# Kernel tuning notes

Hardware: AMD Instinct MI355X
Metric: run time of the kernel (lower is better)

The kernel has to match this reference:

```python
import jax, jax.numpy as jnp
import numpy as np

N_NODES = 100000


def gcn_conv(x, edge_index, W, b):
    """PyG GCNConv: linear transform, add self-loops, sym-normalized scatter-add, bias."""
    n = x.shape[0]
    h = x @ W  # [N, out]
    loop = jnp.arange(n, dtype=edge_index.dtype)
    src = jnp.concatenate([edge_index[0], loop])
    dst = jnp.concatenate([edge_index[1], loop])
    deg = jax.ops.segment_sum(jnp.ones_like(dst, dtype=h.dtype), dst, num_segments=n)
    dinv = jnp.where(deg > 0, jax.lax.rsqrt(jnp.maximum(deg, 1.0)), 0.0)
    norm = dinv[src] * dinv[dst]  # [E+N]
    msg = norm[:, None] * h[src]  # gather + scale
    out = jax.ops.segment_sum(msg, dst, num_segments=n)  # scatter-add
    return out + b


def setup_inputs() -> dict:
    key = jax.random.key(0)
    k1, k2, k3, k4 = jax.random.split(key, 4)
    in_f, gnn_f, out_f = 128, 64, 40
    n_edges = 1600000
    x = jax.random.normal(k1, (N_NODES, in_f), dtype=jnp.float32)
    edge_index = jax.random.randint(k2, (2, n_edges), 0, N_NODES, dtype=jnp.int64)
    W1 = jax.random.normal(k3, (in_f, gnn_f), dtype=jnp.float32) * (in_f ** -0.5)
    b1 = jnp.zeros((gnn_f,), dtype=jnp.float32)
    W2 = jax.random.normal(k4, (gnn_f, out_f), dtype=jnp.float32) * (gnn_f ** -0.5)
    b2 = jnp.zeros((out_f,), dtype=jnp.float32)
    return {"x": x, "edge_index": edge_index, "W1": W1, "b1": b1, "W2": W2, "b2": b2}


def reference(x, edge_index, W1, b1, W2, b2):
    h = gcn_conv(x, edge_index, W1, b1)
    h = jax.nn.relu(h)  # Dropout is identity in eval mode
    out = gcn_conv(h, edge_index, W2, b2)
    return out
```

## Files before the change

### kernel.cpp

```cpp
#include <hip/hip_runtime.h>


__device__ inline float bflo(unsigned u) { return __uint_as_float(u << 16); }
__device__ inline float bfhi(unsigned u) { return __uint_as_float(u & 0xffff0000u); }
__device__ inline unsigned short f2bf(float x) {
    unsigned u = __float_as_uint(x);
    return (unsigned short)((u + 0x7fff + ((u >> 16) & 1)) >> 16);
}

#define NBINS 256
#define EPB   2048

__global__ __launch_bounds__(256) void p1_hist(const int* __restrict__ dst, int e,
                                               int nblk, int* __restrict__ hist_t) {
    __shared__ int h[NBINS];
    int tid = threadIdx.x;
    h[tid] = 0;
    __syncthreads();
    int base = blockIdx.x * EPB;
    #pragma unroll
    for (int j = 0; j < 8; ++j) {
        int idx = base + j * 256 + tid;
        if (idx < e) atomicAdd(&h[dst[idx] >> 9], 1);
    }
    __syncthreads();
    hist_t[tid * nblk + blockIdx.x] = h[tid];
}

__global__ __launch_bounds__(256) void scan_a(const int* __restrict__ in, int* __restrict__ part,
                                              int* __restrict__ aux, int n) {
    __shared__ int lds[256];
    int tid = threadIdx.x;
    int base = blockIdx.x * 1024 + tid * 4;
    int v0 = (base + 0 < n) ? in[base + 0] : 0;
    int v1 = (base + 1 < n) ? in[base + 1] : 0;
    int v2 = (base + 2 < n) ? in[base + 2] : 0;
    int v3 = (base + 3 < n) ? in[base + 3] : 0;
    int s = v0 + v1 + v2 + v3;
    lds[tid] = s;
    __syncthreads();
    for (int off = 1; off < 256; off <<= 1) {
        int t = (tid >= off) ? lds[tid - off] : 0;
        __syncthreads();
        lds[tid] += t;
        __syncthreads();
    }
    int excl = lds[tid] - s;
    if (base + 0 < n) part[base + 0] = excl;
    if (base + 1 < n) part[base + 1] = excl + v0;
    if (base + 2 < n) part[base + 2] = excl + v0 + v1;
    if (base + 3 < n) part[base + 3] = excl + v0 + v1 + v2;
    if (tid == 255) aux[blockIdx.x] = lds[255];
}

__global__ __launch_bounds__(256) void scan_b(int* __restrict__ aux, int nb) {
    __shared__ int lds[256];
    int tid = threadIdx.x;
    int v = (tid < nb) ? aux[tid] : 0;
    lds[tid] = v;
    __syncthreads();
    for (int off = 1; off < 256; off <<= 1) {
        int t = (tid >= off) ? lds[tid - off] : 0;
        __syncthreads();
        lds[tid] += t;
        __syncthreads();
    }
    if (tid < nb) aux[tid] = lds[tid] - v;
}

__global__ __launch_bounds__(256) void scan_c(int* __restrict__ data,
                                              const int* __restrict__ aux, int n) {
    int i = blockIdx.x * blockDim.x + threadIdx.x;
    if (i < n) data[i] += aux[i >> 10];
}

__global__ __launch_bounds__(256) void p1_scatter(const int* __restrict__ src,
                                                  const int* __restrict__ dst, int e,
                                                  int nblk, const int* __restrict__ off_t,
                                                  uint2* __restrict__ ebuf) {
    __shared__ int cur[NBINS];
    int tid = threadIdx.x;
    cur[tid] = off_t[tid * nblk + blockIdx.x];
    __syncthreads();
    int base = blockIdx.x * EPB;
    #pragma unroll
    for (int j = 0; j < 8; ++j) {
        int idx = base + j * 256 + tid;
        if (idx < e) {
            int d = dst[idx];
            int p = atomicAdd(&cur[d >> 9], 1);
            ebuf[p] = make_uint2((unsigned)src[idx], (unsigned)d);
        }
    }
}

__global__ __launch_bounds__(256) void p2_build(const uint2* __restrict__ ebuf,
                                                const int* __restrict__ off_t,
                                                int nblk, int e, int n, int nbg,
                                                int* __restrict__ row_off,
                                                int* __restrict__ ssrc,
                                                float* __restrict__ dinv) {
    __shared__ int cnt[512];
    __shared__ int s1[256];
    __shared__ int loc[512];
    int tid = threadIdx.x;
    int g = blockIdx.x;
    int node0 = g << 9;
    int nlocal = n - node0; if (nlocal > 512) nlocal = 512;

    int segstart = off_t[g * nblk];
    int segend   = (g + 1 < NBINS) ? off_t[(g + 1) * nblk] : e;

    cnt[tid] = 0; cnt[tid + 256] = 0;
    __syncthreads();

    for (int i = segstart + tid; i < segend; i += 256)
        atomicAdd(&cnt[ebuf[i].y - node0], 1);
    __syncthreads();

    int a0 = cnt[2 * tid], a1 = cnt[2 * tid + 1];
    int sp = a0 + a1;
    s1[tid] = sp;
    __syncthreads();
    for (int off = 1; off < 256; off <<= 1) {
        int t = (tid >= off) ? s1[tid - off] : 0;
        __syncthreads();
        s1[tid] += t;
        __syncthreads();
    }
    int excl = s1[tid] - sp;
    loc[2 * tid]     = excl;
    loc[2 * tid + 1] = excl + a0;
    __syncthreads();

    for (int l = tid; l < nlocal; l += 256) {
        row_off[node0 + l] = segstart + loc[l];
        dinv[node0 + l] = rsqrtf((float)cnt[l] + 1.0f);
    }
    if (g == nbg - 1 && tid == 0) row_off[n] = segend;
    __syncthreads();

    for (int i = segstart + tid; i < segend; i += 256) {
        uint2 p = ebuf[i];
        int r = atomicAdd(&loc[p.y - node0], 1);
        ssrc[segstart + r] = (int)p.x;
    }
}

template <int K, int M>
__global__ __launch_bounds__(256) void gemm_xw(const float* __restrict__ X,
                                               const float* __restrict__ W,
                                               const float* __restrict__ dinv,
                                               unsigned short* __restrict__ G, int n) {
    constexpr int KQ = K / 4;
    constexpr int SG = KQ + 1;
    __shared__ float4 xs[64 * SG];
    __shared__ float4 wt[64 * SG];

    const int tid = threadIdx.x;
    const int r0  = blockIdx.x * 64;

    for (int idx = tid; idx < 64 * KQ; idx += 256) {
        int m  = idx / KQ;
        int kq = idx & (KQ - 1);
        float4 v = make_float4(0.f, 0.f, 0.f, 0.f);
        if (m < M) {
            int k = kq * 4;
            v.x = W[(k + 0) * M + m];
            v.y = W[(k + 1) * M + m];
            v.z = W[(k + 2) * M + m];
            v.w = W[(k + 3) * M + m];
        }
        wt[m * SG + kq] = v;
    }
    for (int idx = tid; idx < 64 * KQ; idx += 256) {
        int row = idx / KQ;
        int kq  = idx & (KQ - 1);
        int rr  = r0 + row; rr = rr < n ? rr : n - 1;
        xs[row * SG + kq] = *reinterpret_cast<const float4*>(&X[(size_t)rr * K + kq * 4]);
    }
    __syncthreads();

    const int tc = tid & 15;
    const int tr = tid >> 4;

    float acc[4][4];
    #pragma unroll
    for (int i = 0; i < 4; ++i)
        #pragma unroll
        for (int j = 0; j < 4; ++j) acc[i][j] = 0.f;

    #pragma unroll 2
    for (int kq = 0; kq < KQ; ++kq) {
        float4 xv[4], wv[4];
        #pragma unroll
        for (int i = 0; i < 4; ++i) xv[i] = xs[(tr + 16 * i) * SG + kq];
        #pragma unroll
        for (int j = 0; j < 4; ++j) wv[j] = wt[(tc + 16 * j) * SG + kq];
        #pragma unroll
        for (int i = 0; i < 4; ++i)
            #pragma unroll
            for (int j = 0; j < 4; ++j) {
                acc[i][j] = fmaf(xv[i].x, wv[j].x, acc[i][j]);
                acc[i][j] = fmaf(xv[i].y, wv[j].y, acc[i][j]);
                acc[i][j] = fmaf(xv[i].z, wv[j].z, acc[i][j]);
                acc[i][j] = fmaf(xv[i].w, wv[j].w, acc[i][j]);
            }
    }

    #pragma unroll
    for (int i = 0; i < 4; ++i) {
        int row = r0 + tr + 16 * i;
        if (row < n) {
            float di = dinv[row];
            #pragma unroll
            for (int j = 0; j < 4; ++j) {
                int col = tc + 16 * j;
                if (col < M) G[(size_t)row * M + col] = f2bf(di * acc[i][j]);
            }
        }
    }
}

template <bool RELU>
__global__ __launch_bounds__(256) void aggregate64(const unsigned short* __restrict__ G,
                                                   const float* __restrict__ dinv,
                                                   const int* __restrict__ row_off,
                                                   const int* __restrict__ ssrc,
                                                   const float* __restrict__ bias,
                                                   float* __restrict__ out, int n) {
    int wid  = (blockIdx.x * blockDim.x + threadIdx.x) >> 6;
    if (wid >= n) return;
    int lane = threadIdx.x & 63;
    int q = lane >> 4;
    int c = lane & 15;
    const uint2* __restrict__ G4 = (const uint2*)G;

    float4 acc = make_float4(0.f, 0.f, 0.f, 0.f);
    int e0 = row_off[wid], e1 = row_off[wid + 1];

    int e = e0 + q;
    for (; e + 4 < e1; e += 8) {
        int s0 = ssrc[e], s1 = ssrc[e + 4];
        uint2 g0 = G4[(size_t)s0 * 16 + c];
        uint2 g1 = G4[(size_t)s1 * 16 + c];
        acc.x += bflo(g0.x); acc.y += bfhi(g0.x); acc.z += bflo(g0.y); acc.w += bfhi(g0.y);
        acc.x += bflo(g1.x); acc.y += bfhi(g1.x); acc.z += bflo(g1.y); acc.w += bfhi(g1.y);
    }
    if (e < e1) {
        int s = ssrc[e];
        uint2 g = G4[(size_t)s * 16 + c];
        acc.x += bflo(g.x); acc.y += bfhi(g.x); acc.z += bflo(g.y); acc.w += bfhi(g.y);
    }

    acc.x += __shfl_xor(acc.x, 16); acc.y += __shfl_xor(acc.y, 16);
    acc.z += __shfl_xor(acc.z, 16); acc.w += __shfl_xor(acc.w, 16);
    acc.x += __shfl_xor(acc.x, 32); acc.y += __shfl_xor(acc.y, 32);
    acc.z += __shfl_xor(acc.z, 32); acc.w += __shfl_xor(acc.w, 32);

    float di = dinv[wid];
    uint2 gs = G4[(size_t)wid * 16 + c];
    float4 bv = ((const float4*)bias)[c];
    float4 o;
    o.x = fmaf(di, acc.x + bflo(gs.x), bv.x);
    o.y = fmaf(di, acc.y + bfhi(gs.x), bv.y);
    o.z = fmaf(di, acc.z + bflo(gs.y), bv.z);
    o.w = fmaf(di, acc.w + bfhi(gs.y), bv.w);
    if (RELU) {
        o.x = fmaxf(o.x, 0.f); o.y = fmaxf(o.y, 0.f);
        o.z = fmaxf(o.z, 0.f); o.w = fmaxf(o.w, 0.f);
    }
    if (q == 0) ((float4*)out)[(size_t)wid * 16 + c] = o;
}

template <bool RELU>
__global__ __launch_bounds__(256) void aggregate40(const unsigned short* __restrict__ G,
                                                   const float* __restrict__ dinv,
                                                   const int* __restrict__ row_off,
                                                   const int* __restrict__ ssrc,
                                                   const float* __restrict__ bias,
                                                   float* __restrict__ out, int n) {
    constexpr int MH = 20;
    int wid  = (blockIdx.x * blockDim.x + threadIdx.x) >> 6;
    if (wid >= n) return;
    int lane = threadIdx.x & 63;
    int half = lane >> 5;
    int c    = lane & 31;
    int cc   = c < MH ? c : MH - 1;
    const unsigned* __restrict__ G2 = (const unsigned*)G;

    float2 acc = make_float2(0.f, 0.f);
    int e0 = row_off[wid], e1 = row_off[wid + 1];

    int e = e0 + half;
    for (; e + 2 < e1; e += 4) {
        int s0 = ssrc[e], s1 = ssrc[e + 2];
        unsigned g0 = G2[(size_t)s0 * MH + cc];
        unsigned g1 = G2[(size_t)s1 * MH + cc];
        acc.x += bflo(g0); acc.y += bfhi(g0);
        acc.x += bflo(g1); acc.y += bfhi(g1);
    }
    if (e < e1) {
        unsigned g = G2[(size_t)ssrc[e] * MH + cc];
        acc.x += bflo(g); acc.y += bfhi(g);
    }

    acc.x += __shfl_xor(acc.x, 32);
    acc.y += __shfl_xor(acc.y, 32);

    float di = dinv[wid];
    unsigned gs = G2[(size_t)wid * MH + cc];
    float2 bv = ((const float2*)bias)[cc];
    float o0 = fmaf(di, acc.x + bflo(gs), bv.x);
    float o1 = fmaf(di, acc.y + bfhi(gs), bv.y);
    if (RELU) { o0 = fmaxf(o0, 0.f); o1 = fmaxf(o1, 0.f); }
    if (half == 0 && c < MH) {
        ((float2*)out)[(size_t)wid * MH + c] = make_float2(o0, o1);
    }
}

extern "C" void kernel_launch(void* const* d_in, const int* in_sizes, int n_in,
                              void* d_out, int out_size, void* d_ws, size_t ws_size,
                              hipStream_t stream) {
    const float* x  = (const float*)d_in[0];
    const int*   ei = (const int*)d_in[1];
    const float* W1 = (const float*)d_in[2];
    const float* b1 = (const float*)d_in[3];
    const float* W2 = (const float*)d_in[4];
    const float* b2 = (const float*)d_in[5];

    const int gnn_f = in_sizes[3];
    const int out_f = in_sizes[5];
    const int in_f  = in_sizes[2] / gnn_f;
    const int e     = in_sizes[1] / 2;
    const int n     = in_sizes[0] / in_f;

    const int* src = ei;
    const int* dst = ei + e;

    const int nblk   = (e + EPB - 1) / EPB;
    const int nscan  = NBINS * nblk;
    const int nbg    = (n + 511) / 512;
    const int nchunks = (nscan + 1023) / 1024;

    char* base = (char*)d_ws;
    size_t off = 0;
    auto alloc = [&](size_t bytes) -> char* {
        char* p = base + off;
        off = (off + bytes + 255) & ~(size_t)255;
        return p;
    };
    int*            hist_t  = (int*)            alloc((size_t)nscan * 4);
    int*            off_t   = (int*)            alloc((size_t)nscan * 4);
    int*            aux     = (int*)            alloc(256 * 4);
    uint2*          ebuf    = (uint2*)          alloc((size_t)e * 8);
    int*            row_off = (int*)            alloc((size_t)(n + 1) * 4);
    int*            ssrc    = (int*)            alloc((size_t)e * 4);
    float*          dinv    = (float*)          alloc((size_t)n * 4);
    unsigned short* g1      = (unsigned short*) alloc((size_t)n * gnn_f * 2);
    float*          a1      = (float*)          alloc((size_t)n * gnn_f * 4);
    unsigned short* g2      = (unsigned short*) alloc((size_t)n * out_f * 2);
    (void)ws_size;

    p1_hist<<<nblk, 256, 0, stream>>>(dst, e, nblk, hist_t);
    scan_a<<<nchunks, 256, 0, stream>>>(hist_t, off_t, aux, nscan);
    scan_b<<<1, 256, 0, stream>>>(aux, nchunks);
    scan_c<<<(nscan + 255) / 256, 256, 0, stream>>>(off_t, aux, nscan);
    p1_scatter<<<nblk, 256, 0, stream>>>(src, dst, e, nblk, off_t, ebuf);
    p2_build<<<nbg, 256, 0, stream>>>(ebuf, off_t, nblk, e, n, nbg, row_off, ssrc, dinv);

    gemm_xw<128, 64><<<(n + 63) / 64, 256, 0, stream>>>(x, W1, dinv, g1, n);
    aggregate64<true><<<(n + 3) / 4, 256, 0, stream>>>(g1, dinv, row_off, ssrc, b1, a1, n);

    gemm_xw<64, 40><<<(n + 63) / 64, 256, 0, stream>>>(a1, W2, dinv, g2, n);
    aggregate40<false><<<(n + 3) / 4, 256, 0, stream>>>(g2, dinv, row_off, ssrc, b2, (float*)d_out, n);
}
```

Before: 322.6 us.

## Pack edge buffer to 32 bits and widen aggregation gathers

The intermediate edge buffer now stores each edge as one 32-bit word: a 17-bit source index plus the destination's 9-bit offset within its 512-node bin. This halves the buffer's write and read traffic. The 64-wide aggregation switches from 8-byte to 16-byte gathers, with eight edges in flight per wavefront and an extra shuffle stage. The 40-wide aggregation unrolls its gather loop to four loads per iteration. The packing assumes node ids below 2^17, which holds for the 100000-node test graph but limits generality.

```diff
diff --git a/kernel.cpp b/kernel.cpp
--- a/kernel.cpp
+++ b/kernel.cpp
@@ -77,7 +77,7 @@
 __global__ __launch_bounds__(256) void p1_scatter(const int* __restrict__ src,
                                                   const int* __restrict__ dst, int e,
                                                   int nblk, const int* __restrict__ off_t,
-                                                  uint2* __restrict__ ebuf) {
+                                                  unsigned* __restrict__ ebuf) {
     __shared__ int cur[NBINS];
     int tid = threadIdx.x;
     cur[tid] = off_t[tid * nblk + blockIdx.x];
@@ -89,12 +89,12 @@
         if (idx < e) {
             int d = dst[idx];
             int p = atomicAdd(&cur[d >> 9], 1);
-            ebuf[p] = make_uint2((unsigned)src[idx], (unsigned)d);
+            ebuf[p] = (unsigned)src[idx] | ((unsigned)(d & 511) << 17);
         }
     }
 }
 
-__global__ __launch_bounds__(256) void p2_build(const uint2* __restrict__ ebuf,
+__global__ __launch_bounds__(256) void p2_build(const unsigned* __restrict__ ebuf,
                                                 const int* __restrict__ off_t,
                                                 int nblk, int e, int n, int nbg,
                                                 int* __restrict__ row_off,
@@ -115,7 +115,7 @@
     __syncthreads();
 
     for (int i = segstart + tid; i < segend; i += 256)
-        atomicAdd(&cnt[ebuf[i].y - node0], 1);
+        atomicAdd(&cnt[ebuf[i] >> 17], 1);
     __syncthreads();
 
     int a0 = cnt[2 * tid], a1 = cnt[2 * tid + 1];
@@ -141,9 +141,9 @@
     __syncthreads();
 
     for (int i = segstart + tid; i < segend; i += 256) {
-        uint2 p = ebuf[i];
-        int r = atomicAdd(&loc[p.y - node0], 1);
-        ssrc[segstart + r] = (int)p.x;
+        unsigned p = ebuf[i];
+        int r = atomicAdd(&loc[p >> 17], 1);
+        ssrc[segstart + r] = (int)(p & 0x1FFFFu);
     }
 }
 
@@ -232,45 +232,68 @@
     int wid  = (blockIdx.x * blockDim.x + threadIdx.x) >> 6;
     if (wid >= n) return;
     int lane = threadIdx.x & 63;
-    int q = lane >> 4;
-    int c = lane & 15;
-    const uint2* __restrict__ G4 = (const uint2*)G;
-
-    float4 acc = make_float4(0.f, 0.f, 0.f, 0.f);
+    int g = lane >> 3;
+    int c = lane & 7;
+    const uint4* __restrict__ G16 = (const uint4*)G;
+
+    float acc[8];
+    #pragma unroll
+    for (int k = 0; k < 8; ++k) acc[k] = 0.f;
+
     int e0 = row_off[wid], e1 = row_off[wid + 1];
-
-    int e = e0 + q;
-    for (; e + 4 < e1; e += 8) {
-        int s0 = ssrc[e], s1 = ssrc[e + 4];
-        uint2 g0 = G4[(size_t)s0 * 16 + c];
-        uint2 g1 = G4[(size_t)s1 * 16 + c];
-        acc.x += bflo(g0.x); acc.y += bfhi(g0.x); acc.z += bflo(g0.y); acc.w += bfhi(g0.y);
-        acc.x += bflo(g1.x); acc.y += bfhi(g1.x); acc.z += bflo(g1.y); acc.w += bfhi(g1.y);
+    int e = e0 + g;
+    for (; e + 8 < e1; e += 16) {
+        int s0 = ssrc[e], s1 = ssrc[e + 8];
+        uint4 u0 = G16[(size_t)s0 * 8 + c];
+        uint4 u1 = G16[(size_t)s1 * 8 + c];
+        acc[0] += bflo(u0.x); acc[1] += bfhi(u0.x);
+        acc[2] += bflo(u0.y); acc[3] += bfhi(u0.y);
+        acc[4] += bflo(u0.z); acc[5] += bfhi(u0.z);
+        acc[6] += bflo(u0.w); acc[7] += bfhi(u0.w);
+        acc[0] += bflo(u1.x); acc[1] += bfhi(u1.x);
+        acc[2] += bflo(u1.y); acc[3] += bfhi(u1.y);
+        acc[4] += bflo(u1.z); acc[5] += bfhi(u1.z);
+        acc[6] += bflo(u1.w); acc[7] += bfhi(u1.w);
     }
     if (e < e1) {
         int s = ssrc[e];
-        uint2 g = G4[(size_t)s * 16 + c];
-        acc.x += bflo(g.x); acc.y += bfhi(g.x); acc.z += bflo(g.y); acc.w += bfhi(g.y);
-    }
-
-    acc.x += __shfl_xor(acc.x, 16); acc.y += __shfl_xor(acc.y, 16);
-    acc.z += __shfl_xor(acc.z, 16); acc.w += __shfl_xor(acc.w, 16);
-    acc.x += __shfl_xor(acc.x, 32); acc.y += __shfl_xor(acc.y, 32);
-    acc.z += __shfl_xor(acc.z, 32); acc.w += __shfl_xor(acc.w, 32);
+        uint4 u = G16[(size_t)s * 8 + c];
+        acc[0] += bflo(u.x); acc[1] += bfhi(u.x);
+        acc[2] += bflo(u.y); acc[3] += bfhi(u.y);
+        acc[4] += bflo(u.z); acc[5] += bfhi(u.z);
+        acc[6] += bflo(u.w); acc[7] += bfhi(u.w);
+    }
+
+    #pragma unroll
+    for (int k = 0; k < 8; ++k) acc[k] += __shfl_xor(acc[k], 8);
+    #pragma unroll
+    for (int k = 0; k < 8; ++k) acc[k] += __shfl_xor(acc[k], 16);
+    #pragma unroll
+    for (int k = 0; k < 8; ++k) acc[k] += __shfl_xor(acc[k], 32);
 
     float di = dinv[wid];
-    uint2 gs = G4[(size_t)wid * 16 + c];
-    float4 bv = ((const float4*)bias)[c];
-    float4 o;
-    o.x = fmaf(di, acc.x + bflo(gs.x), bv.x);
-    o.y = fmaf(di, acc.y + bfhi(gs.x), bv.y);
-    o.z = fmaf(di, acc.z + bflo(gs.y), bv.z);
-    o.w = fmaf(di, acc.w + bfhi(gs.y), bv.w);
+    uint4 gs = G16[(size_t)wid * 8 + c];
+    float4 b0 = ((const float4*)bias)[2 * c];
+    float4 b1 = ((const float4*)bias)[2 * c + 1];
+    float4 o0, o1;
+    o0.x = fmaf(di, acc[0] + bflo(gs.x), b0.x);
+    o0.y = fmaf(di, acc[1] + bfhi(gs.x), b0.y);
+    o0.z = fmaf(di, acc[2] + bflo(gs.y), b0.z);
+    o0.w = fmaf(di, acc[3] + bfhi(gs.y), b0.w);
+    o1.x = fmaf(di, acc[4] + bflo(gs.z), b1.x);
+    o1.y = fmaf(di, acc[5] + bfhi(gs.z), b1.y);
+    o1.z = fmaf(di, acc[6] + bflo(gs.w), b1.z);
+    o1.w = fmaf(di, acc[7] + bfhi(gs.w), b1.w);
     if (RELU) {
-        o.x = fmaxf(o.x, 0.f); o.y = fmaxf(o.y, 0.f);
-        o.z = fmaxf(o.z, 0.f); o.w = fmaxf(o.w, 0.f);
-    }
-    if (q == 0) ((float4*)out)[(size_t)wid * 16 + c] = o;
+        o0.x = fmaxf(o0.x, 0.f); o0.y = fmaxf(o0.y, 0.f);
+        o0.z = fmaxf(o0.z, 0.f); o0.w = fmaxf(o0.w, 0.f);
+        o1.x = fmaxf(o1.x, 0.f); o1.y = fmaxf(o1.y, 0.f);
+        o1.z = fmaxf(o1.z, 0.f); o1.w = fmaxf(o1.w, 0.f);
+    }
+    if (g == 0) {
+        ((float4*)out)[(size_t)wid * 16 + 2 * c]     = o0;
+        ((float4*)out)[(size_t)wid * 16 + 2 * c + 1] = o1;
+    }
 }
 
 template <bool RELU>
@@ -293,14 +316,18 @@
     int e0 = row_off[wid], e1 = row_off[wid + 1];
 
     int e = e0 + half;
-    for (; e + 2 < e1; e += 4) {
-        int s0 = ssrc[e], s1 = ssrc[e + 2];
+    for (; e + 6 < e1; e += 8) {
+        int s0 = ssrc[e], s1 = ssrc[e + 2], s2 = ssrc[e + 4], s3 = ssrc[e + 6];
         unsigned g0 = G2[(size_t)s0 * MH + cc];
         unsigned g1 = G2[(size_t)s1 * MH + cc];
+        unsigned g2 = G2[(size_t)s2 * MH + cc];
+        unsigned g3 = G2[(size_t)s3 * MH + cc];
         acc.x += bflo(g0); acc.y += bfhi(g0);
         acc.x += bflo(g1); acc.y += bfhi(g1);
-    }
-    if (e < e1) {
+        acc.x += bflo(g2); acc.y += bfhi(g2);
+        acc.x += bflo(g3); acc.y += bfhi(g3);
+    }
+    for (; e < e1; e += 2) {
         unsigned g = G2[(size_t)ssrc[e] * MH + cc];
         acc.x += bflo(g); acc.y += bfhi(g);
     }
@@ -353,7 +380,7 @@
     int*            hist_t  = (int*)            alloc((size_t)nscan * 4);
     int*            off_t   = (int*)            alloc((size_t)nscan * 4);
     int*            aux     = (int*)            alloc(256 * 4);
-    uint2*          ebuf    = (uint2*)          alloc((size_t)e * 8);
+    unsigned*       ebuf    = (unsigned*)       alloc((size_t)e * 4);
     int*            row_off = (int*)            alloc((size_t)(n + 1) * 4);
     int*            ssrc    = (int*)            alloc((size_t)e * 4);
     float*          dinv    = (float*)          alloc((size_t)n * 4);
```

Measured after the change: 307.5 us. 1.05x faster.
